# Kernel optimization log

Hardware: AMD Instinct MI355X
Metric: run time of the kernel (lower is better)

## Reference

```python
import jax, jax.numpy as jnp
import numpy as np

B, L = 4096, 64          # batch, patch_len
OUT, KS, K = 64, 8, 4    # out_planes, kernel_size, num mixtures
STRIDE = 1
TEMP = 34.0
L_OUT = (L - KS) // STRIDE + 1   # 57
C = OUT * L_OUT                  # BN feature dim = 3648
HIDDEN = int(L * 0.5) + 1        # attention hidden planes = 33
EPS = 1e-5


def _gelu(x):
    return jax.nn.gelu(x, approximate=False)  # torch nn.GELU default = exact erf


def setup_inputs() -> dict:
    key = jax.random.key(0)
    ks = jax.random.split(key, 8)
    return {
        "x": jax.random.normal(ks[0], (B, L), jnp.float32),
        "fc1_w": jax.random.normal(ks[1], (HIDDEN, L), jnp.float32) * (2.0 / HIDDEN) ** 0.5,
        "fc2_w": jax.random.normal(ks[2], (K, HIDDEN), jnp.float32) * (2.0 / K) ** 0.5,
        "fc2_b": jnp.zeros((K,), jnp.float32),
        "weight": jax.random.normal(ks[3], (K, OUT, KS), jnp.float32) * 0.1,
        "bias": jnp.zeros((K, OUT), jnp.float32),
        "bn_gamma": jnp.ones((C,), jnp.float32),
        "bn_beta": jnp.zeros((C,), jnp.float32),
    }


def reference(x, fc1_w, fc2_w, fc2_b, weight, bias, bn_gamma, bn_beta):
    # --- attention1d: 1x1 convs over the patch_len 'channel' dim == linears ---
    a = _gelu(x @ fc1_w.T)                 # [B, HIDDEN]
    logits = a @ fc2_w.T + fc2_b           # [B, K]
    attn = jax.nn.softmax(logits / TEMP, axis=1)

    # --- sliding windows (im2col), shared by both conv paths ---
    idx = jnp.arange(L_OUT)[:, None] * STRIDE + jnp.arange(KS)[None, :]
    frames = x[:, idx]                     # [B, L_OUT, KS]

    # --- kernel_wise: full conv with each of the K kernels ---
    kw = jnp.einsum('blc,koc->bolk', frames, weight) + bias.T[None, :, None, :]  # [B,OUT,L_OUT,K]
    kw = kw.reshape(B, C, K)

    # --- per-sample aggregated kernel + grouped (per-sample) conv ---
    agg_w = jnp.einsum('bk,koc->boc', attn, weight)      # [B, OUT, KS]
    agg_b = attn @ bias                                  # [B, OUT]
    out = jnp.einsum('blc,boc->bol', frames, agg_w) + agg_b[:, :, None]  # [B,OUT,L_OUT]
    out = out.reshape(B, C)

    # --- BN(GELU(.)) with batch statistics (training-mode BatchNorm1d) ---
    g = _gelu(out)
    m = g.mean(axis=0)
    v = g.var(axis=0)
    out = (g - m) * jax.lax.rsqrt(v + EPS) * bn_gamma + bn_beta

    g2 = _gelu(kw)                                        # [B, C, K]
    m2 = g2.mean(axis=(0, 2), keepdims=True)
    v2 = g2.var(axis=(0, 2), keepdims=True)
    kw = (g2 - m2) * jax.lax.rsqrt(v2 + EPS) * bn_gamma[None, :, None] + bn_beta[None, :, None]

    return out, attn, kw.transpose(0, 2, 1)              # [B,C], [B,K], [B,K,C]
```

## Files before the change

kernel.cpp:

```cpp
#include <hip/hip_runtime.h>
#include <cstddef>

#define B_     4096
#define L_     64
#define OUT_   64
#define KS_    8
#define KK_    4
#define LOUT_  57
#define C_     3648
#define HID_   33
#define TEMP_  34.0f
#define EPS_   1e-5f
#define NCH_   64
#define SROWS_ 32
#define NB2_   32

__device__ __forceinline__ float gelu_f(float x) {
    float u = x * fmaf(0.044715f * x, x, 1.0f) * 1.5957691216f;
    float e = __expf(-u);
    return x * __builtin_amdgcn_rcpf(1.0f + e);
}

__global__ __launch_bounds__(128) void attn_kernel(
    const float* __restrict__ x, const float* __restrict__ fc1_w,
    const float* __restrict__ fc2_w, const float* __restrict__ fc2_b,
    float* __restrict__ attn_out)
{
    __shared__ float fc1s[HID_][L_];
    __shared__ float fc2s[KK_][HID_];
    __shared__ float fc2bs[KK_];
    int tid = threadIdx.x;
    for (int i = tid; i < HID_ * L_; i += 128) fc1s[i / L_][i % L_] = fc1_w[i];
    for (int i = tid; i < KK_ * HID_; i += 128) fc2s[i / HID_][i % HID_] = fc2_w[i];
    if (tid < KK_) fc2bs[tid] = fc2_b[tid];
    __syncthreads();

    int b = blockIdx.x * 128 + tid;
    if (b >= B_) return;

    float xr[L_];
    const float4* xp = (const float4*)(x + (size_t)b * L_);
    #pragma unroll
    for (int i = 0; i < L_ / 4; ++i) {
        float4 v = xp[i];
        xr[4*i] = v.x; xr[4*i+1] = v.y; xr[4*i+2] = v.z; xr[4*i+3] = v.w;
    }
    float logit[KK_] = {0.f, 0.f, 0.f, 0.f};
    for (int h = 0; h < HID_; ++h) {
        const float4* fr = (const float4*)&fc1s[h][0];
        float acc = 0.f;
        #pragma unroll
        for (int i = 0; i < L_ / 4; ++i) {
            float4 wv = fr[i];
            acc = fmaf(xr[4*i],   wv.x, acc);
            acc = fmaf(xr[4*i+1], wv.y, acc);
            acc = fmaf(xr[4*i+2], wv.z, acc);
            acc = fmaf(xr[4*i+3], wv.w, acc);
        }
        float a = gelu_f(acc);
        #pragma unroll
        for (int k = 0; k < KK_; ++k) logit[k] = fmaf(a, fc2s[k][h], logit[k]);
    }
    float z[KK_];
    #pragma unroll
    for (int k = 0; k < KK_; ++k) z[k] = (logit[k] + fc2bs[k]) * (1.0f / TEMP_);
    float mx = fmaxf(fmaxf(z[0], z[1]), fmaxf(z[2], z[3]));
    float e[KK_]; float s = 0.f;
    #pragma unroll
    for (int k = 0; k < KK_; ++k) { e[k] = __expf(z[k] - mx); s += e[k]; }
    float inv = __builtin_amdgcn_rcpf(s);
    #pragma unroll
    for (int k = 0; k < KK_; ++k) attn_out[(size_t)b * KK_ + k] = e[k] * inv;
}

__global__ __launch_bounds__(256) void stats_kernel(
    const float* __restrict__ x, const float* __restrict__ weight,
    const float* __restrict__ bias, const float* __restrict__ attn,
    float* __restrict__ P, int use_partial)
{
    const int RPC = B_ / NCH_;
    int cb = blockIdx.x;
    int chunk = blockIdx.y;
    int tid = threadIdx.x;
    int c = cb * 256 + tid;
    bool act = c < C_;
    int o = act ? (c / LOUT_) : 0;
    int l = act ? (c - o * LOUT_) : 0;

    float w[KK_][KS_];
    float bk[KK_];
    #pragma unroll
    for (int k = 0; k < KK_; ++k) {
        bk[k] = bias[k * OUT_ + o];
        #pragma unroll
        for (int cq = 0; cq < KS_; ++cq) w[k][cq] = weight[(k * OUT_ + o) * KS_ + cq];
    }

    __shared__ float xs[SROWS_][L_];
    __shared__ float at[SROWS_][KK_];

    float s1 = 0.f, s2 = 0.f, t1 = 0.f, t2 = 0.f;

    for (int round = 0; round < RPC / SROWS_; ++round) {
        int b0 = chunk * RPC + round * SROWS_;
        __syncthreads();
        {
            const float4* xp4 = (const float4*)(x + (size_t)b0 * L_);
            float4* xd = (float4*)&xs[0][0];
            xd[tid] = xp4[tid];
            xd[tid + 256] = xp4[tid + 256];
            if (tid < SROWS_ * KK_) ((float*)at)[tid] = attn[(size_t)b0 * KK_ + tid];
        }
        __syncthreads();
        if (act) {
            #pragma unroll 4
            for (int r = 0; r < SROWS_; ++r) {
                float kv0 = bk[0], kv1 = bk[1], kv2 = bk[2], kv3 = bk[3];
                #pragma unroll
                for (int cq = 0; cq < KS_; ++cq) {
                    float xv = xs[r][l + cq];
                    kv0 = fmaf(xv, w[0][cq], kv0);
                    kv1 = fmaf(xv, w[1][cq], kv1);
                    kv2 = fmaf(xv, w[2][cq], kv2);
                    kv3 = fmaf(xv, w[3][cq], kv3);
                }
                float ov = at[r][0] * kv0;
                ov = fmaf(at[r][1], kv1, ov);
                ov = fmaf(at[r][2], kv2, ov);
                ov = fmaf(at[r][3], kv3, ov);
                float g = gelu_f(ov);
                s1 += g; s2 = fmaf(g, g, s2);
                float g0 = gelu_f(kv0), g1 = gelu_f(kv1), g2 = gelu_f(kv2), g3 = gelu_f(kv3);
                t1 += g0 + g1 + g2 + g3;
                t2 = fmaf(g0, g0, t2); t2 = fmaf(g1, g1, t2);
                t2 = fmaf(g2, g2, t2); t2 = fmaf(g3, g3, t2);
            }
        }
    }
    if (!act) return;
    if (use_partial) {
        size_t base = (size_t)chunk * 4 * C_ + c;
        P[base]          = s1;
        P[base + C_]     = s2;
        P[base + 2 * C_] = t1;
        P[base + 3 * C_] = t2;
    } else {
        atomicAdd(&P[c], s1);
        atomicAdd(&P[C_ + c], s2);
        atomicAdd(&P[2 * C_ + c], t1);
        atomicAdd(&P[3 * C_ + c], t2);
    }
}

__global__ __launch_bounds__(256) void finalize_kernel(
    const float* __restrict__ P, const float* __restrict__ gamma,
    const float* __restrict__ beta, float* __restrict__ F, int use_partial)
{
    int c = blockIdx.x * 256 + threadIdx.x;
    if (c >= C_) return;
    float a0, a1, a2, a3;
    if (use_partial) {
        a0 = a1 = a2 = a3 = 0.f;
        for (int ch = 0; ch < NCH_; ++ch) {
            size_t base = (size_t)ch * 4 * C_ + c;
            a0 += P[base];
            a1 += P[base + C_];
            a2 += P[base + 2 * C_];
            a3 += P[base + 3 * C_];
        }
    } else {
        a0 = P[c]; a1 = P[C_ + c]; a2 = P[2 * C_ + c]; a3 = P[3 * C_ + c];
    }
    float m  = a0 * (1.0f / B_);
    float v  = a1 * (1.0f / B_) - m * m;
    float rs = rsqrtf(v + EPS_);
    float m2 = a2 * (1.0f / (B_ * KK_));
    float v2 = a3 * (1.0f / (B_ * KK_)) - m2 * m2;
    float rs2 = rsqrtf(v2 + EPS_);
    float ga = gamma[c], be = beta[c];
    F[c]          = rs * ga;
    F[C_ + c]     = be - m * rs * ga;
    F[2 * C_ + c] = rs2 * ga;
    F[3 * C_ + c] = be - m2 * rs2 * ga;
}

__global__ __launch_bounds__(256) void write_kernel(
    const float* __restrict__ x, const float* __restrict__ weight,
    const float* __restrict__ bias, const float* __restrict__ attn,
    const float* __restrict__ F,
    float* __restrict__ out0, float* __restrict__ kwout)
{
    int cc = blockIdx.x;
    int bg = blockIdx.y;
    int tid = threadIdx.x;
    int c = cc * 256 + tid;
    bool act = c < C_;
    int o = act ? (c / LOUT_) : 0;
    int l = act ? (c - o * LOUT_) : 0;

    float w[KK_][KS_];
    float bk[KK_];
    #pragma unroll
    for (int k = 0; k < KK_; ++k) {
        bk[k] = bias[k * OUT_ + o];
        #pragma unroll
        for (int cq = 0; cq < KS_; ++cq) w[k][cq] = weight[(k * OUT_ + o) * KS_ + cq];
    }
    float sA = 0.f, hA = 0.f, sK = 0.f, hK = 0.f;
    if (act) {
        sA = F[c]; hA = F[C_ + c]; sK = F[2 * C_ + c]; hK = F[3 * C_ + c];
    }

    __shared__ float xs[NB2_][L_];
    __shared__ float at[NB2_][KK_];
    int b0 = bg * NB2_;
    {
        const float4* xp4 = (const float4*)(x + (size_t)b0 * L_);
        float4* xd = (float4*)&xs[0][0];
        xd[tid] = xp4[tid];
        xd[tid + 256] = xp4[tid + 256];
        if (tid < NB2_ * KK_) ((float*)at)[tid] = attn[(size_t)b0 * KK_ + tid];
    }
    __syncthreads();

    if (!act) return;

    #pragma unroll 4
    for (int r = 0; r < NB2_; ++r) {
        float kv0 = bk[0], kv1 = bk[1], kv2 = bk[2], kv3 = bk[3];
        #pragma unroll
        for (int cq = 0; cq < KS_; ++cq) {
            float xv = xs[r][l + cq];
            kv0 = fmaf(xv, w[0][cq], kv0);
            kv1 = fmaf(xv, w[1][cq], kv1);
            kv2 = fmaf(xv, w[2][cq], kv2);
            kv3 = fmaf(xv, w[3][cq], kv3);
        }
        float ov = at[r][0] * kv0;
        ov = fmaf(at[r][1], kv1, ov);
        ov = fmaf(at[r][2], kv2, ov);
        ov = fmaf(at[r][3], kv3, ov);
        int b = b0 + r;
        float g = gelu_f(ov);
        __builtin_nontemporal_store(fmaf(g, sA, hA), &out0[(size_t)b * C_ + c]);
        float g0 = gelu_f(kv0), g1 = gelu_f(kv1), g2v = gelu_f(kv2), g3 = gelu_f(kv3);
        float* base = kwout + (size_t)b * KK_ * C_ + c;
        __builtin_nontemporal_store(fmaf(g0,  sK, hK), base);
        __builtin_nontemporal_store(fmaf(g1,  sK, hK), base + C_);
        __builtin_nontemporal_store(fmaf(g2v, sK, hK), base + 2 * C_);
        __builtin_nontemporal_store(fmaf(g3,  sK, hK), base + 3 * C_);
    }
}

extern "C" void kernel_launch(void* const* d_in, const int* in_sizes, int n_in,
                              void* d_out, int out_size, void* d_ws, size_t ws_size,
                              hipStream_t stream) {
    const float* x      = (const float*)d_in[0];
    const float* fc1_w  = (const float*)d_in[1];
    const float* fc2_w  = (const float*)d_in[2];
    const float* fc2_b  = (const float*)d_in[3];
    const float* weight = (const float*)d_in[4];
    const float* bias   = (const float*)d_in[5];
    const float* gamma  = (const float*)d_in[6];
    const float* beta   = (const float*)d_in[7];

    float* out  = (float*)d_out;
    float* out0 = out;
    float* attn = out + (size_t)B_ * C_;
    float* kwout = attn + (size_t)B_ * KK_;

    size_t need = (size_t)(NCH_ * 4 + 4) * C_ * sizeof(float);
    int use_partial = ws_size >= need;
    float* P = (float*)d_ws;
    float* F = P + (use_partial ? (size_t)NCH_ * 4 * C_ : (size_t)4 * C_);
    if (!use_partial)
        hipMemsetAsync(P, 0, 4 * C_ * sizeof(float), stream);

    attn_kernel<<<B_ / 128, 128, 0, stream>>>(x, fc1_w, fc2_w, fc2_b, attn);
    stats_kernel<<<dim3((C_ + 255) / 256, NCH_), 256, 0, stream>>>(
        x, weight, bias, attn, P, use_partial);
    finalize_kernel<<<(C_ + 255) / 256, 256, 0, stream>>>(P, gamma, beta, F, use_partial);
    write_kernel<<<dim3((C_ + 255) / 256, B_ / NB2_), 256, 0, stream>>>(
        x, weight, bias, attn, F, out0, kwout);
}
```

Measured before the change: 152.3 us.

## Double stats chunks, parallelize finalize, simplify GELU exp, drop nontemporal stores

Raises the number of batch chunks in the stats pass so more blocks run concurrently. The finalize kernel now gives each of the four statistics its own group of 64 threads and combines them through shared memory, instead of one thread looping serially over all chunks. GELU folds its constants into a single exp2 call, and the output writes go back to ordinary stores instead of nontemporal ones. Doubling the chunks doubles the partial-sum workspace and the reads finalize has to do, and normal stores may change cache behaviour on the large output writes.

```diff
diff --git a/kernel.cpp b/kernel.cpp
--- a/kernel.cpp
+++ b/kernel.cpp
@@ -11,13 +11,12 @@
 #define HID_   33
 #define TEMP_  34.0f
 #define EPS_   1e-5f
-#define NCH_   64
+#define NCH_   128
 #define SROWS_ 32
 #define NB2_   32
 
 __device__ __forceinline__ float gelu_f(float x) {
-    float u = x * fmaf(0.044715f * x, x, 1.0f) * 1.5957691216f;
-    float e = __expf(-u);
+    float e = exp2f(-2.3022083f * x * fmaf(0.044715f * x, x, 1.0f));
     return x * __builtin_amdgcn_rcpf(1.0f + e);
 }
 
@@ -156,32 +155,34 @@
     const float* __restrict__ P, const float* __restrict__ gamma,
     const float* __restrict__ beta, float* __restrict__ F, int use_partial)
 {
-    int c = blockIdx.x * 256 + threadIdx.x;
-    if (c >= C_) return;
-    float a0, a1, a2, a3;
+    __shared__ float red[4][64];
+    int t = threadIdx.x;
+    int cl = t & 63;
+    int s = t >> 6;
+    int c = blockIdx.x * 64 + cl;
+    float a = 0.f;
     if (use_partial) {
-        a0 = a1 = a2 = a3 = 0.f;
-        for (int ch = 0; ch < NCH_; ++ch) {
-            size_t base = (size_t)ch * 4 * C_ + c;
-            a0 += P[base];
-            a1 += P[base + C_];
-            a2 += P[base + 2 * C_];
-            a3 += P[base + 3 * C_];
-        }
+        for (int ch = 0; ch < NCH_; ++ch)
+            a += P[((size_t)ch * 4 + s) * C_ + c];
     } else {
-        a0 = P[c]; a1 = P[C_ + c]; a2 = P[2 * C_ + c]; a3 = P[3 * C_ + c];
-    }
-    float m  = a0 * (1.0f / B_);
-    float v  = a1 * (1.0f / B_) - m * m;
-    float rs = rsqrtf(v + EPS_);
-    float m2 = a2 * (1.0f / (B_ * KK_));
-    float v2 = a3 * (1.0f / (B_ * KK_)) - m2 * m2;
-    float rs2 = rsqrtf(v2 + EPS_);
-    float ga = gamma[c], be = beta[c];
-    F[c]          = rs * ga;
-    F[C_ + c]     = be - m * rs * ga;
-    F[2 * C_ + c] = rs2 * ga;
-    F[3 * C_ + c] = be - m2 * rs2 * ga;
+        a = P[(size_t)s * C_ + c];
+    }
+    red[s][cl] = a;
+    __syncthreads();
+    if (t < 64) {
+        float a0 = red[0][cl], a1 = red[1][cl], a2 = red[2][cl], a3 = red[3][cl];
+        float m  = a0 * (1.0f / B_);
+        float v  = a1 * (1.0f / B_) - m * m;
+        float rs = rsqrtf(v + EPS_);
+        float m2 = a2 * (1.0f / (B_ * KK_));
+        float v2 = a3 * (1.0f / (B_ * KK_)) - m2 * m2;
+        float rs2 = rsqrtf(v2 + EPS_);
+        float ga = gamma[c], be = beta[c];
+        F[c]          = rs * ga;
+        F[C_ + c]     = be - m * rs * ga;
+        F[2 * C_ + c] = rs2 * ga;
+        F[3 * C_ + c] = be - m2 * rs2 * ga;
+    }
 }
 
 __global__ __launch_bounds__(256) void write_kernel(
@@ -242,13 +243,13 @@
         ov = fmaf(at[r][3], kv3, ov);
         int b = b0 + r;
         float g = gelu_f(ov);
-        __builtin_nontemporal_store(fmaf(g, sA, hA), &out0[(size_t)b * C_ + c]);
+        out0[(size_t)b * C_ + c] = fmaf(g, sA, hA);
         float g0 = gelu_f(kv0), g1 = gelu_f(kv1), g2v = gelu_f(kv2), g3 = gelu_f(kv3);
         float* base = kwout + (size_t)b * KK_ * C_ + c;
-        __builtin_nontemporal_store(fmaf(g0,  sK, hK), base);
-        __builtin_nontemporal_store(fmaf(g1,  sK, hK), base + C_);
-        __builtin_nontemporal_store(fmaf(g2v, sK, hK), base + 2 * C_);
-        __builtin_nontemporal_store(fmaf(g3,  sK, hK), base + 3 * C_);
+        base[0]      = fmaf(g0,  sK, hK);
+        base[C_]     = fmaf(g1,  sK, hK);
+        base[2 * C_] = fmaf(g2v, sK, hK);
+        base[3 * C_] = fmaf(g3,  sK, hK);
     }
 }
 
@@ -279,7 +280,7 @@
     attn_kernel<<<B_ / 128, 128, 0, stream>>>(x, fc1_w, fc2_w, fc2_b, attn);
     stats_kernel<<<dim3((C_ + 255) / 256, NCH_), 256, 0, stream>>>(
         x, weight, bias, attn, P, use_partial);
-    finalize_kernel<<<(C_ + 255) / 256, 256, 0, stream>>>(P, gamma, beta, F, use_partial);
+    finalize_kernel<<<C_ / 64, 256, 0, stream>>>(P, gamma, beta, F, use_partial);
     write_kernel<<<dim3((C_ + 255) / 256, B_ / NB2_), 256, 0, stream>>>(
         x, weight, bias, attn, F, out0, kwout);
 }
```

Measured after the change: 147.2 us. 1.03x faster.
